# Optimization experiments

Measured on AMD Instinct MI355X. Metric: run time of the kernel, lower is better.

## Reference

```python
import jax, jax.numpy as jnp
import numpy as np

EMBED_DIM = 1024
NUM_HEADS = 16
HEAD_DIM = EMBED_DIM // NUM_HEADS


def setup_inputs() -> dict:
    key = jax.random.key(0)
    k_x, k_wqkv, k_bqkv, k_wp, k_bp = jax.random.split(key, 5)
    B, S = 4, 2048
    scale = 1.0 / np.sqrt(EMBED_DIM)
    return {
        "x": jax.random.normal(k_x, (B, S, EMBED_DIM), dtype=jnp.float32),
        # torch nn.Linear stores weight as [out_features, in_features]
        "w_qkv": jax.random.uniform(k_wqkv, (3 * EMBED_DIM, EMBED_DIM), dtype=jnp.float32, minval=-scale, maxval=scale),
        "b_qkv": jax.random.uniform(k_bqkv, (3 * EMBED_DIM,), dtype=jnp.float32, minval=-scale, maxval=scale),
        "w_proj": jax.random.uniform(k_wp, (EMBED_DIM, EMBED_DIM), dtype=jnp.float32, minval=-scale, maxval=scale),
        "b_proj": jax.random.uniform(k_bp, (EMBED_DIM,), dtype=jnp.float32, minval=-scale, maxval=scale),
    }


def reference(x, w_qkv, b_qkv, w_proj, b_proj):
    B, S, _ = x.shape
    # qkv projection: [B,S,3E]
    qkv = jnp.einsum('bse,fe->bsf', x, w_qkv) + b_qkv
    qkv = qkv.reshape(B, S, 3, NUM_HEADS, HEAD_DIM)
    qkv = jnp.transpose(qkv, (2, 0, 3, 1, 4))  # [3,B,H,S,Dh]
    q, k, v = qkv[0], qkv[1], qkv[2]
    # scaled dot-product attention (no mask, eval-mode dropout = identity)
    scores = jnp.einsum('bhqd,bhkd->bhqk', q, k) / np.sqrt(HEAD_DIM)
    attn = jax.nn.softmax(scores, axis=-1)
    out = jnp.einsum('bhqk,bhkd->bhqd', attn, v)  # [B,H,S,Dh]
    out = jnp.transpose(out, (0, 2, 1, 3)).reshape(B, S, EMBED_DIM)
    return jnp.einsum('bse,fe->bsf', out, w_proj) + b_proj
```

## Files before the change

kernel.cpp:

```cpp
#include <hip/hip_runtime.h>

#define EDIM 1024
#define NHEADS 16
#define HDIM 64
#define SEQ 2048
#define BATCH 4
#define MROWS (BATCH * SEQ)
#define NQKV (3 * EDIM)
#define QKB 2048

typedef __attribute__((ext_vector_type(4))) float f32x4;
typedef __attribute__((ext_vector_type(8))) short s16x8;
typedef __attribute__((ext_vector_type(4))) short s16x4;
typedef __attribute__((ext_vector_type(4))) unsigned int u32x4;

#define AS1 __attribute__((address_space(1)))
#define AS3 __attribute__((address_space(3)))
#define GLOAD_LDS16(g, l) __builtin_amdgcn_global_load_lds( \
    (AS1 void*)(void*)(g), (AS3 void*)(void*)(l), 16, 0, 0)

static __device__ __forceinline__ unsigned short f2bf(float f) {
  unsigned int u = __builtin_bit_cast(unsigned int, f);
  u += 0x7fffu + ((u >> 16) & 1u);
  return (unsigned short)(u >> 16);
}

static __device__ __forceinline__ float fexp2(float x) {
  float r;
  asm("v_exp_f32 %0, %1" : "=v"(r) : "v"(x));
  return r;
}

static __device__ __forceinline__ unsigned int cvtpk(float a, float b) {
  unsigned int r;
  asm("v_cvt_pk_bf16_f32 %0, %1, %2" : "=v"(r) : "v"(a), "v"(b));
  return r;
}

static __device__ __forceinline__ f32x4 mfma_bf16(s16x8 a, s16x8 b, f32x4 c) {
  return __builtin_amdgcn_mfma_f32_16x16x32_bf16(a, b, c, 0, 0, 0);
}

template <int N>
static __device__ __forceinline__ void wait_vm() {
  if constexpr (N >= 8)      asm volatile("s_waitcnt lgkmcnt(0) vmcnt(8)" ::: "memory");
  else if constexpr (N == 6) asm volatile("s_waitcnt lgkmcnt(0) vmcnt(6)" ::: "memory");
  else if constexpr (N == 4) asm volatile("s_waitcnt lgkmcnt(0) vmcnt(4)" ::: "memory");
  else if constexpr (N == 3) asm volatile("s_waitcnt lgkmcnt(0) vmcnt(3)" ::: "memory");
  else                       asm volatile("s_waitcnt lgkmcnt(0) vmcnt(0)" ::: "memory");
}

__global__ void __launch_bounds__(256) cvt_all(const float* __restrict__ x,
                                               const float* __restrict__ wq,
                                               const float* __restrict__ wp,
                                               unsigned short* __restrict__ out) {
  const int i = blockIdx.x * 256 + threadIdx.x;
  const float* src;
  int j;
  if (i < 2097152) { src = x;  j = i; }
  else if (i < 2883584) { src = wq; j = i - 2097152; }
  else { src = wp; j = i - 2883584; }
  const float4 v = ((const float4*)src)[j];
  ushort4 o;
  o.x = f2bf(v.x); o.y = f2bf(v.y); o.z = f2bf(v.z); o.w = f2bf(v.w);
  ((ushort4*)out)[i] = o;
}

template <int MODE, int BMP, int BNP>
__global__ void __launch_bounds__(512, 2) gemm256(const unsigned short* __restrict__ Ap,
                                                  const unsigned short* __restrict__ Bp,
                                                  const float* __restrict__ bias,
                                                  void* __restrict__ Cout,
                                                  int M, int N, int K) {
  extern __shared__ unsigned short lds[];
  constexpr int ASLOT = BMP * 4096;
  constexpr int BSLOT = BNP * 4096;
  constexpr int BBASE = 4 * ASLOT;
  constexpr int L = BMP + BNP;

  const int tid = threadIdx.x;
  const int lane = tid & 63;
  const int wave = tid >> 6;
  const int wr = wave >> 2;
  const int wc = wave & 3;
  const int lr = lane & 15, kg = lane >> 4;

  const int nwg = gridDim.x;
  const int q8 = nwg >> 3;
  const int wgid = (blockIdx.x & 7) * q8 + (blockIdx.x >> 3);
  const int NBM = M >> (BMP == 2 ? 8 : 7);
  const long m0 = (long)(wgid % NBM) * (BMP * 128);
  const long n0 = (long)(wgid / NBM) * (BNP * 128);

#define STAGE(slot, kt) do {                                                   \
    _Pragma("unroll")                                                          \
    for (int i_ = 0; i_ < BMP; ++i_) {                                         \
      const int c_ = wave * BMP + i_;                \
      const int r_ = c_ * 16 + (lane >> 2);                                    \
      const int sc_ = ((lane & 3) ^ ((r_ >> 1) & 3)) * 8;                      \
      GLOAD_LDS16(Ap + (m0 + r_) * K + (kt) * 32 + sc_,                        \
                  &lds[(slot) * ASLOT + c_ * 512]);                            \
    }                                                                          \
    _Pragma("unroll")                                                          \
    for (int i_ = 0; i_ < BNP; ++i_) {                                         \
      const int c_ = wave * BNP + i_;                                          \
      const int r_ = c_ * 16 + (lane >> 2);                                    \
      const int sc_ = ((lane & 3) ^ ((r_ >> 1) & 3)) * 8;                      \
      GLOAD_LDS16(Bp + (n0 + r_) * K + (kt) * 32 + sc_,                        \
                  &lds[BBASE + (slot) * BSLOT + c_ * 512]);                    \
    }                                                                          \
  } while (0)

  f32x4 acc[BMP * 4][BNP * 2] = {};
  const int nk = K >> 5;

  STAGE(0, 0); STAGE(1, 1); STAGE(2, 2);
  wait_vm<2 * L>();
  __builtin_amdgcn_s_barrier();
  __builtin_amdgcn_sched_barrier(0);

  for (int t = 0; t < nk; ++t) {
    if (t + 3 < nk) STAGE((t + 3) & 3, t + 3);

    const unsigned short* Asl = &lds[(t & 3) * ASLOT];
    const unsigned short* Bsl = &lds[BBASE + (t & 3) * BSLOT];
    s16x8 af[BMP * 4], bf[BNP * 2];
#pragma unroll
    for (int mt = 0; mt < BMP * 4; ++mt) {
      const int r = wr * (BMP * 64) + mt * 16 + lr;
      af[mt] = *(const s16x8*)&Asl[r * 32 + ((kg * 8) ^ (((r >> 1) & 3) << 3))];
    }
#pragma unroll
    for (int nt = 0; nt < BNP * 2; ++nt) {
      const int r = wc * (BNP * 32) + nt * 16 + lr;
      bf[nt] = *(const s16x8*)&Bsl[r * 32 + ((kg * 8) ^ (((r >> 1) & 3) << 3))];
    }
    __builtin_amdgcn_s_setprio(1);
#pragma unroll
    for (int mt = 0; mt < BMP * 4; ++mt)
#pragma unroll
      for (int nt = 0; nt < BNP * 2; ++nt)
        acc[mt][nt] = mfma_bf16(af[mt], bf[nt], acc[mt][nt]);
    __builtin_amdgcn_s_setprio(0);

    if (t + 1 < nk) {
      if (t + 3 < nk)      wait_vm<2 * L>();
      else if (t + 2 < nk) wait_vm<L>();
      else                 wait_vm<0>();
      __builtin_amdgcn_s_barrier();
      __builtin_amdgcn_sched_barrier(0);
    }
  }

#pragma unroll
  for (int nt = 0; nt < BNP * 2; ++nt) {
    const long col = n0 + wc * (BNP * 32) + nt * 16 + lr;
    const float bv = (MODE == 2) ? 0.f : bias[col];
#pragma unroll
    for (int mt = 0; mt < BMP * 4; ++mt) {
#pragma unroll
      for (int r = 0; r < 4; ++r) {
        const long row = m0 + wr * (BMP * 64) + mt * 16 + kg * 4 + r;
        if (MODE == 0) {
          float v = acc[mt][nt][r] + bv;
          if (col < EDIM) v *= 0.18033688011112042f;
          ((unsigned short*)Cout)[row * QKB + col] = f2bf(v);
        } else if (MODE == 1) {
          ((float*)Cout)[row * N + col] = acc[mt][nt][r] + bv;
        } else {
          const float v = acc[mt][nt][r] + bias[row];
          ((unsigned short*)Cout)[((col >> 11) * 1024 + row) * (long)2048 +
                                  (col & 2047)] = f2bf(v);
        }
      }
    }
  }
#undef STAGE
}

template <int BUF>
static __device__ __forceinline__ void attn_tile(
    const unsigned short (&Ks)[2][2][4096],
    const unsigned short (&Vs)[2][2][4096],
    const s16x8 (&qf)[2][2],
    f32x4 (&o_acc)[2][4],
    f32x4 (&l_part)[2],
    const int lr, const int kg) {
  unsigned int pk[2][2][4][2];
#pragma unroll
  for (int hh = 0; hh < 2; ++hh) {
    f32x4 st[2][4];
    __builtin_amdgcn_s_setprio(1);
#pragma unroll
    for (int ct = 0; ct < 4; ++ct) {
      const int rb = (ct * 16 + lr) * 128;
      const int sw = (lr & 7) << 4;
      const s16x8 k0 = *(const s16x8*)&Ks[BUF][hh][(rb + ((kg * 16) ^ sw)) >> 1];
      const s16x8 k1 = *(const s16x8*)&Ks[BUF][hh][(rb + ((64 + kg * 16) ^ sw)) >> 1];
#pragma unroll
      for (int qs = 0; qs < 2; ++qs) {
        f32x4 a = {};
        a = mfma_bf16(k0, qf[qs][0], a);
        a = mfma_bf16(k1, qf[qs][1], a);
        st[qs][ct] = a;
      }
    }
    __builtin_amdgcn_s_setprio(0);
#pragma unroll
    for (int qs = 0; qs < 2; ++qs) {
      f32x4 rv = {0.f, 0.f, 0.f, 0.f};
#pragma unroll
      for (int ct = 0; ct < 4; ++ct) {
        f32x4 p;
#pragma unroll
        for (int r = 0; r < 4; ++r) p[r] = fexp2(st[qs][ct][r]);
        rv += p;
        pk[qs][hh][ct][0] = cvtpk(p[0], p[1]);
        pk[qs][hh][ct][1] = cvtpk(p[2], p[3]);
      }
      l_part[qs] += rv;
    }
  }
#pragma unroll
  for (int hh = 0; hh < 2; ++hh) {
#pragma unroll
    for (int kc = 0; kc < 2; ++kc) {
      s16x8 pa[2];
#pragma unroll
      for (int qs = 0; qs < 2; ++qs) {
        u32x4 wv = {pk[qs][hh][2 * kc][0], pk[qs][hh][2 * kc][1],
                    pk[qs][hh][2 * kc + 1][0], pk[qs][hh][2 * kc + 1][1]};
        pa[qs] = __builtin_bit_cast(s16x8, wv);
      }
      __builtin_amdgcn_s_setprio(1);
#pragma unroll
      for (int dt = 0; dt < 4; ++dt) {
        const int rb = (dt * 16 + lr) * 128;
        const int c0 = (64 * kc + 8 * kg) ^ ((lr & 7) << 4);
        const s16x4 v0 = *(const s16x4*)&Vs[BUF][hh][(rb + c0) >> 1];
        const s16x4 v1 = *(const s16x4*)&Vs[BUF][hh][(rb + (c0 ^ 32)) >> 1];
        const s16x8 vf = __builtin_shufflevector(v0, v1, 0, 1, 2, 3, 4, 5, 6, 7);
#pragma unroll
        for (int qs = 0; qs < 2; ++qs)
          o_acc[qs][dt] = mfma_bf16(pa[qs], vf, o_acc[qs][dt]);
      }
      __builtin_amdgcn_s_setprio(0);
    }
  }
}

__global__ void __launch_bounds__(256, 2) attn_fwd(const unsigned short* __restrict__ qk,
                                                   const unsigned short* __restrict__ vT,
                                                   unsigned short* __restrict__ attout) {
  const int L = blockIdx.x;
  const int bh = (L & 7) * 8 + ((L >> 3) >> 4);
  const int qt = (L >> 3) & 15;
  const int b = bh >> 4, h = bh & 15;
  const int q0 = qt * 128;
  const int tid = threadIdx.x, lane = tid & 63, wave = tid >> 6;
  const int lr = lane & 15, kg = lane >> 4;

  __shared__ unsigned short Ks[2][2][4096];
  __shared__ unsigned short Vs[2][2][4096];

  const long rowbase = (long)b * SEQ;

#define STAGE(BUF, kv0) do {                                                     \
    _Pragma("unroll")                                                            \
    for (int hh_ = 0; hh_ < 2; ++hh_) {                                          \
      _Pragma("unroll")                                                          \
      for (int i_ = 0; i_ < 2; ++i_) {                                           \
        const int c_ = wave * 2 + i_;                                            \
        const int row_ = c_ * 8 + (lane >> 3);                                   \
        const int col_ = ((lane & 7) ^ (lane >> 3)) << 3;                        \
        GLOAD_LDS16(qk + (rowbase + (kv0) + hh_ * 64 + row_) * QKB + EDIM +      \
                        h * HDIM + col_,                                         \
                    &Ks[BUF][hh_][c_ * 512]);                                    \
        GLOAD_LDS16(vT + ((long)bh * HDIM + row_) * SEQ + (kv0) + hh_ * 64 +     \
                        col_,                                                    \
                    &Vs[BUF][hh_][c_ * 512]);                                    \
      }                                                                          \
    }                                                                            \
  } while (0)

  s16x8 qf[2][2];
#pragma unroll
  for (int qs = 0; qs < 2; ++qs) {
    const unsigned short* qp =
        qk + (rowbase + q0 + wave * 32 + qs * 16 + lr) * QKB + h * HDIM + kg * 8;
    qf[qs][0] = *(const s16x8*)qp;
    qf[qs][1] = *(const s16x8*)(qp + 32);
  }

  f32x4 l_part[2] = {{0.f, 0.f, 0.f, 0.f}, {0.f, 0.f, 0.f, 0.f}};
  f32x4 o_acc[2][4] = {};

  STAGE(0, 0);
  __syncthreads();

  for (int kv0 = 0; kv0 < SEQ; kv0 += 256) {
    STAGE(1, kv0 + 128);
    attn_tile<0>(Ks, Vs, qf, o_acc, l_part, lr, kg);
    __syncthreads();
    if (kv0 + 256 < SEQ) STAGE(0, kv0 + 256);
    attn_tile<1>(Ks, Vs, qf, o_acc, l_part, lr, kg);
    __syncthreads();
  }

#pragma unroll
  for (int qs = 0; qs < 2; ++qs) {
    float rs = (l_part[qs][0] + l_part[qs][1]) + (l_part[qs][2] + l_part[qs][3]);
    rs += __shfl_xor(rs, 16, 64);
    rs += __shfl_xor(rs, 32, 64);
#pragma unroll
    for (int r = 0; r < 4; ++r) {
      const float lq = __shfl(rs, kg * 4 + r, 64);
      const float inv = 1.0f / lq;
      const long row = rowbase + q0 + wave * 32 + qs * 16 + kg * 4 + r;
#pragma unroll
      for (int dt = 0; dt < 4; ++dt)
        attout[row * EDIM + h * HDIM + dt * 16 + lr] = f2bf(o_acc[qs][dt][r] * inv);
    }
  }
#undef STAGE
}

extern "C" void kernel_launch(void* const* d_in, const int* in_sizes, int n_in,
                              void* d_out, int out_size, void* d_ws, size_t ws_size,
                              hipStream_t stream) {
  const float* x      = (const float*)d_in[0];
  const float* w_qkv  = (const float*)d_in[1];
  const float* b_qkv  = (const float*)d_in[2];
  const float* w_proj = (const float*)d_in[3];
  const float* b_proj = (const float*)d_in[4];

  unsigned short* xb   = (unsigned short*)d_ws;
  unsigned short* wqb  = xb   + (size_t)MROWS * EDIM;
  unsigned short* wpb  = wqb  + (size_t)NQKV * EDIM;
  unsigned short* qkb  = wpb  + (size_t)EDIM * EDIM;
  unsigned short* attb = qkb  + (size_t)MROWS * QKB;
  unsigned short* vTb  = attb + (size_t)MROWS * EDIM;

  const int sh22 = 131072;
  const int sh12 = 98304;
  const int sh21 = 98304;
  hipFuncSetAttribute((const void*)gemm256<0, 2, 2>,
                      hipFuncAttributeMaxDynamicSharedMemorySize, sh22);
  hipFuncSetAttribute((const void*)gemm256<2, 1, 2>,
                      hipFuncAttributeMaxDynamicSharedMemorySize, sh12);
  hipFuncSetAttribute((const void*)gemm256<1, 2, 1>,
                      hipFuncAttributeMaxDynamicSharedMemorySize, sh21);

  cvt_all<<<12288, 256, 0, stream>>>(x, w_qkv, w_proj, xb);

  gemm256<0, 2, 2><<<(MROWS / 256) * (QKB / 256), 512, sh22, stream>>>(
      xb, wqb, b_qkv, qkb, MROWS, QKB, EDIM);

  gemm256<2, 1, 2><<<(EDIM / 128) * (MROWS / 256), 512, sh12, stream>>>(
      wqb + (size_t)2048 * EDIM, xb, b_qkv + 2048, vTb, EDIM, MROWS, EDIM);

  attn_fwd<<<1024, 256, 0, stream>>>(qkb, vTb, attb);

  gemm256<1, 2, 1><<<(MROWS / 256) * (EDIM / 128), 512, sh21, stream>>>(
      attb, wpb, b_proj, d_out, MROWS, EDIM, EDIM);
}
```

Measured before the change: 192.6 us.

## Restructure attention into 512-thread blocks with 4-slot 64-row KV pipeline

The attention kernel now uses 8 waves per block covering 256 query rows, so each K/V tile staged in LDS is shared by twice as many queries. The old double buffer of 128-row KV tiles becomes a 4-slot ring of 64-row tiles kept three tiles ahead. Each step waits with partial vmcnt waits and a raw s_barrier instead of a full __syncthreads. The goal is to halve global K/V traffic per query and keep loads in flight across compute. The cost is fewer blocks (512) and tighter per-wave register and occupancy limits under launch_bounds(512,4).

```diff
diff --git a/kernel.cpp b/kernel.cpp
--- a/kernel.cpp
+++ b/kernel.cpp
@@ -47,6 +47,7 @@
   else if constexpr (N == 6) asm volatile("s_waitcnt lgkmcnt(0) vmcnt(6)" ::: "memory");
   else if constexpr (N == 4) asm volatile("s_waitcnt lgkmcnt(0) vmcnt(4)" ::: "memory");
   else if constexpr (N == 3) asm volatile("s_waitcnt lgkmcnt(0) vmcnt(3)" ::: "memory");
+  else if constexpr (N == 2) asm volatile("s_waitcnt lgkmcnt(0) vmcnt(2)" ::: "memory");
   else                       asm volatile("s_waitcnt lgkmcnt(0) vmcnt(0)" ::: "memory");
 }
 
@@ -178,25 +179,62 @@
 #undef STAGE
 }
 
-template <int BUF>
-static __device__ __forceinline__ void attn_tile(
-    const unsigned short (&Ks)[2][2][4096],
-    const unsigned short (&Vs)[2][2][4096],
-    const s16x8 (&qf)[2][2],
-    f32x4 (&o_acc)[2][4],
-    f32x4 (&l_part)[2],
-    const int lr, const int kg) {
-  unsigned int pk[2][2][4][2];
-#pragma unroll
-  for (int hh = 0; hh < 2; ++hh) {
+__global__ void __launch_bounds__(512, 4) attn_fwd(const unsigned short* __restrict__ qk,
+                                                   const unsigned short* __restrict__ vT,
+                                                   unsigned short* __restrict__ attout) {
+  const int L = blockIdx.x;
+  const int bh = (L & 7) * 8 + (L >> 6);
+  const int qt = (L >> 3) & 7;
+  const int b = bh >> 4, h = bh & 15;
+  const int q0 = qt * 256;
+  const int tid = threadIdx.x, lane = tid & 63, wave = tid >> 6;
+  const int lr = lane & 15, kg = lane >> 4;
+
+  __shared__ unsigned short Ks[4][4096];
+  __shared__ unsigned short Vs[4][4096];
+
+  const long rowbase = (long)b * SEQ;
+
+#define ASTAGE(slot, kv0) do {                                                  \
+    const int row_ = wave * 8 + (lane >> 3);                                    \
+    const int col_ = ((lane & 7) ^ (lane >> 3)) << 3;                           \
+    GLOAD_LDS16(qk + (rowbase + (kv0) + row_) * QKB + EDIM + h * HDIM + col_,   \
+                &Ks[slot][wave * 512]);                                         \
+    GLOAD_LDS16(vT + ((long)bh * HDIM + row_) * SEQ + (kv0) + col_,             \
+                &Vs[slot][wave * 512]);                                         \
+  } while (0)
+
+  s16x8 qf[2][2];
+#pragma unroll
+  for (int qs = 0; qs < 2; ++qs) {
+    const unsigned short* qp =
+        qk + (rowbase + q0 + wave * 32 + qs * 16 + lr) * QKB + h * HDIM + kg * 8;
+    qf[qs][0] = *(const s16x8*)qp;
+    qf[qs][1] = *(const s16x8*)(qp + 32);
+  }
+
+  f32x4 l_part[2] = {{0.f, 0.f, 0.f, 0.f}, {0.f, 0.f, 0.f, 0.f}};
+  f32x4 o_acc[2][4] = {};
+
+  ASTAGE(0, 0); ASTAGE(1, 64); ASTAGE(2, 128);
+  wait_vm<4>();
+  __builtin_amdgcn_s_barrier();
+  __builtin_amdgcn_sched_barrier(0);
+
+  for (int t = 0; t < 32; ++t) {
+    if (t + 3 < 32) ASTAGE((t + 3) & 3, (t + 3) * 64);
+
+    const unsigned short* Kb = Ks[t & 3];
+    const unsigned short* Vb = Vs[t & 3];
+
     f32x4 st[2][4];
     __builtin_amdgcn_s_setprio(1);
 #pragma unroll
     for (int ct = 0; ct < 4; ++ct) {
       const int rb = (ct * 16 + lr) * 128;
       const int sw = (lr & 7) << 4;
-      const s16x8 k0 = *(const s16x8*)&Ks[BUF][hh][(rb + ((kg * 16) ^ sw)) >> 1];
-      const s16x8 k1 = *(const s16x8*)&Ks[BUF][hh][(rb + ((64 + kg * 16) ^ sw)) >> 1];
+      const s16x8 k0 = *(const s16x8*)&Kb[(rb + ((kg * 16) ^ sw)) >> 1];
+      const s16x8 k1 = *(const s16x8*)&Kb[(rb + ((64 + kg * 16) ^ sw)) >> 1];
 #pragma unroll
       for (int qs = 0; qs < 2; ++qs) {
         f32x4 a = {};
@@ -206,6 +244,8 @@
       }
     }
     __builtin_amdgcn_s_setprio(0);
+
+    unsigned int pk[2][4][2];
 #pragma unroll
     for (int qs = 0; qs < 2; ++qs) {
       f32x4 rv = {0.f, 0.f, 0.f, 0.f};
@@ -215,21 +255,19 @@
 #pragma unroll
         for (int r = 0; r < 4; ++r) p[r] = fexp2(st[qs][ct][r]);
         rv += p;
-        pk[qs][hh][ct][0] = cvtpk(p[0], p[1]);
-        pk[qs][hh][ct][1] = cvtpk(p[2], p[3]);
+        pk[qs][ct][0] = cvtpk(p[0], p[1]);
+        pk[qs][ct][1] = cvtpk(p[2], p[3]);
       }
       l_part[qs] += rv;
     }
-  }
-#pragma unroll
-  for (int hh = 0; hh < 2; ++hh) {
+
 #pragma unroll
     for (int kc = 0; kc < 2; ++kc) {
       s16x8 pa[2];
 #pragma unroll
       for (int qs = 0; qs < 2; ++qs) {
-        u32x4 wv = {pk[qs][hh][2 * kc][0], pk[qs][hh][2 * kc][1],
-                    pk[qs][hh][2 * kc + 1][0], pk[qs][hh][2 * kc + 1][1]};
+        u32x4 wv = {pk[qs][2 * kc][0], pk[qs][2 * kc][1],
+                    pk[qs][2 * kc + 1][0], pk[qs][2 * kc + 1][1]};
         pa[qs] = __builtin_bit_cast(s16x8, wv);
       }
       __builtin_amdgcn_s_setprio(1);
@@ -237,8 +275,8 @@
       for (int dt = 0; dt < 4; ++dt) {
         const int rb = (dt * 16 + lr) * 128;
         const int c0 = (64 * kc + 8 * kg) ^ ((lr & 7) << 4);
-        const s16x4 v0 = *(const s16x4*)&Vs[BUF][hh][(rb + c0) >> 1];
-        const s16x4 v1 = *(const s16x4*)&Vs[BUF][hh][(rb + (c0 ^ 32)) >> 1];
+        const s16x4 v0 = *(const s16x4*)&Vb[(rb + c0) >> 1];
+        const s16x4 v1 = *(const s16x4*)&Vb[(rb + (c0 ^ 32)) >> 1];
         const s16x8 vf = __builtin_shufflevector(v0, v1, 0, 1, 2, 3, 4, 5, 6, 7);
 #pragma unroll
         for (int qs = 0; qs < 2; ++qs)
@@ -246,65 +284,14 @@
       }
       __builtin_amdgcn_s_setprio(0);
     }
-  }
-}
-
-__global__ void __launch_bounds__(256, 2) attn_fwd(const unsigned short* __restrict__ qk,
-                                                   const unsigned short* __restrict__ vT,
-                                                   unsigned short* __restrict__ attout) {
-  const int L = blockIdx.x;
-  const int bh = (L & 7) * 8 + ((L >> 3) >> 4);
-  const int qt = (L >> 3) & 15;
-  const int b = bh >> 4, h = bh & 15;
-  const int q0 = qt * 128;
-  const int tid = threadIdx.x, lane = tid & 63, wave = tid >> 6;
-  const int lr = lane & 15, kg = lane >> 4;
-
-  __shared__ unsigned short Ks[2][2][4096];
-  __shared__ unsigned short Vs[2][2][4096];
-
-  const long rowbase = (long)b * SEQ;
-
-#define STAGE(BUF, kv0) do {                                                     \
-    _Pragma("unroll")                                                            \
-    for (int hh_ = 0; hh_ < 2; ++hh_) {                                          \
-      _Pragma("unroll")                                                          \
-      for (int i_ = 0; i_ < 2; ++i_) {                                           \
-        const int c_ = wave * 2 + i_;                                            \
-        const int row_ = c_ * 8 + (lane >> 3);                                   \
-        const int col_ = ((lane & 7) ^ (lane >> 3)) << 3;                        \
-        GLOAD_LDS16(qk + (rowbase + (kv0) + hh_ * 64 + row_) * QKB + EDIM +      \
-                        h * HDIM + col_,                                         \
-                    &Ks[BUF][hh_][c_ * 512]);                                    \
-        GLOAD_LDS16(vT + ((long)bh * HDIM + row_) * SEQ + (kv0) + hh_ * 64 +     \
-                        col_,                                                    \
-                    &Vs[BUF][hh_][c_ * 512]);                                    \
-      }                                                                          \
-    }                                                                            \
-  } while (0)
-
-  s16x8 qf[2][2];
-#pragma unroll
-  for (int qs = 0; qs < 2; ++qs) {
-    const unsigned short* qp =
-        qk + (rowbase + q0 + wave * 32 + qs * 16 + lr) * QKB + h * HDIM + kg * 8;
-    qf[qs][0] = *(const s16x8*)qp;
-    qf[qs][1] = *(const s16x8*)(qp + 32);
-  }
-
-  f32x4 l_part[2] = {{0.f, 0.f, 0.f, 0.f}, {0.f, 0.f, 0.f, 0.f}};
-  f32x4 o_acc[2][4] = {};
-
-  STAGE(0, 0);
-  __syncthreads();
-
-  for (int kv0 = 0; kv0 < SEQ; kv0 += 256) {
-    STAGE(1, kv0 + 128);
-    attn_tile<0>(Ks, Vs, qf, o_acc, l_part, lr, kg);
-    __syncthreads();
-    if (kv0 + 256 < SEQ) STAGE(0, kv0 + 256);
-    attn_tile<1>(Ks, Vs, qf, o_acc, l_part, lr, kg);
-    __syncthreads();
+
+    if (t + 1 < 32) {
+      if (t + 3 < 32)      wait_vm<4>();
+      else if (t + 2 < 32) wait_vm<2>();
+      else                 wait_vm<0>();
+      __builtin_amdgcn_s_barrier();
+      __builtin_amdgcn_sched_barrier(0);
+    }
   }
 
 #pragma unroll
@@ -322,7 +309,7 @@
         attout[row * EDIM + h * HDIM + dt * 16 + lr] = f2bf(o_acc[qs][dt][r] * inv);
     }
   }
-#undef STAGE
+#undef ASTAGE
 }
 
 extern "C" void kernel_launch(void* const* d_in, const int* in_sizes, int n_in,
@@ -359,7 +346,7 @@
   gemm256<2, 1, 2><<<(EDIM / 128) * (MROWS / 256), 512, sh12, stream>>>(
       wqb + (size_t)2048 * EDIM, xb, b_qkv + 2048, vTb, EDIM, MROWS, EDIM);
 
-  attn_fwd<<<1024, 256, 0, stream>>>(qkb, vTb, attb);
+  attn_fwd<<<512, 512, 0, stream>>>(qkb, vTb, attb);
 
   gemm256<1, 2, 1><<<(MROWS / 256) * (EDIM / 128), 512, sh21, stream>>>(
       attb, wpb, b_proj, d_out, MROWS, EDIM, EDIM);
```

Result: no change. 190.6 us, median of 2 (-1.0%).
